# Optimization experiments

Hardware: AMD Instinct MI355X
Metric: run time of the kernel (lower is better)

## Reference

```python
import jax, jax.numpy as jnp
import numpy as np

N_IN = 200000
N_OUT = 600000
K = 27          # 3x3x3 kernel offsets
P = 150000      # kernel-map pairs per offset
C_IN = 96
C_OUT = 96
BN_EPS = 1e-5


def setup_inputs() -> dict:
    key = jax.random.key(0)
    k1, k2, k3, k4 = jax.random.split(key, 4)
    feats = jax.random.normal(k1, (N_IN, C_IN), dtype=jnp.float32)
    # kernel map: per offset, input-site indices and output-site indices
    in_idx = jax.random.randint(k2, (K, P), 0, N_IN, dtype=jnp.int32)
    out_idx = jax.random.randint(k3, (K, P), 0, N_OUT, dtype=jnp.int32)
    weight = jax.random.normal(k4, (K, C_IN, C_OUT), dtype=jnp.float32) * (1.0 / np.sqrt(C_IN * K))
    gamma = jnp.ones((C_OUT,), dtype=jnp.float32)
    beta = jnp.zeros((C_OUT,), dtype=jnp.float32)
    return {"feats": feats, "in_idx": in_idx, "out_idx": out_idx,
            "weight": weight, "gamma": gamma, "beta": beta}


def reference(feats, in_idx, out_idx, weight, gamma, beta):
    # Sparse transposed conv: gather -> matmul -> scatter-add per kernel offset.
    out = jnp.zeros((N_OUT, C_OUT), dtype=feats.dtype)
    for k in range(K):  # fixed small loop over kernel offsets (structurally distinct weights)
        contrib = feats[in_idx[k]] @ weight[k]          # [P, C_OUT]
        out = out.at[out_idx[k]].add(contrib)
    # BatchNorm (training-mode batch stats over active output sites), per channel
    mean = jnp.mean(out, axis=0)
    var = jnp.mean((out - mean) ** 2, axis=0)
    y = (out - mean) * jax.lax.rsqrt(var + BN_EPS) * gamma + beta
    # ReLU
    return jax.nn.relu(y)
```

## Files before the change

### kernel.cpp

```cpp
#include <hip/hip_runtime.h>
#include <hip/hip_bf16.h>

#define N_IN   200000
#define N_OUT  600000
#define KOFF   27
#define PPAIR  150000
#define NPAIR  (KOFF * PPAIR)
#define C      96
#define BN_EPS 1e-5f

using bf16x8 = __attribute__((ext_vector_type(8))) __bf16;
using f32x4  = __attribute__((ext_vector_type(4))) float;

static __device__ __forceinline__ unsigned short f2b(float x) {
    __hip_bfloat16 h = __float2bfloat16(x);
    return *reinterpret_cast<unsigned short*>(&h);
}

__global__ void cvt_feats(const float* __restrict__ src, unsigned short* __restrict__ dst) {
    int t = blockIdx.x * 256 + threadIdx.x;
    const float4* s4 = (const float4*)src;
    float4 a = s4[2 * t], b = s4[2 * t + 1];
    union { unsigned short u[8]; uint4 v; } r;
    r.u[0] = f2b(a.x); r.u[1] = f2b(a.y); r.u[2] = f2b(a.z); r.u[3] = f2b(a.w);
    r.u[4] = f2b(b.x); r.u[5] = f2b(b.y); r.u[6] = f2b(b.z); r.u[7] = f2b(b.w);
    ((uint4*)dst)[t] = r.v;
}

__global__ void cvt_w(const float* __restrict__ w, unsigned short* __restrict__ wt) {
    int t = blockIdx.x * 256 + threadIdx.x;
    int k = t / 9216;
    int rem = t - k * 9216;
    int o = rem / 96;
    int i = rem - o * 96;
    wt[t] = f2b(w[k * 9216 + i * 96 + o]);
}

__global__ void k_hist(const int* __restrict__ out_idx, int* __restrict__ counts) {
    int t = blockIdx.x * 256 + threadIdx.x;
    if (t < NPAIR) atomicAdd(&counts[out_idx[t]], 1);
}

__global__ void k_bsum(const int* __restrict__ counts, int* __restrict__ bsum) {
    __shared__ int ls[256];
    int b = blockIdx.x, t = threadIdx.x;
    int base = b * 1024 + t * 4;
    int s = 0;
#pragma unroll
    for (int j = 0; j < 4; j++) { int i = base + j; if (i < N_OUT) s += counts[i]; }
    ls[t] = s;
    __syncthreads();
    for (int off = 128; off > 0; off >>= 1) {
        if (t < off) ls[t] += ls[t + off];
        __syncthreads();
    }
    if (t == 0) bsum[b] = ls[0];
}

__global__ void k_scan_bsum(const int* __restrict__ bsum, int* __restrict__ bsum_ex) {
    __shared__ int sc[1024];
    int t = threadIdx.x;
    int v = (t < 586) ? bsum[t] : 0;
    sc[t] = v;
    __syncthreads();
    for (int off = 1; off < 1024; off <<= 1) {
        int add = (t >= off) ? sc[t - off] : 0;
        __syncthreads();
        sc[t] += add;
        __syncthreads();
    }
    bsum_ex[t] = sc[t] - v;
}

__global__ void k_scan_local(const int* __restrict__ counts, const int* __restrict__ bsum_ex,
                             int* __restrict__ csr) {
    __shared__ int sc[256];
    int b = blockIdx.x, t = threadIdx.x;
    int base = b * 1024 + t * 4;
    int c[4];
    int s = 0;
#pragma unroll
    for (int j = 0; j < 4; j++) {
        int i = base + j;
        c[j] = (i < N_OUT) ? counts[i] : 0;
        s += c[j];
    }
    sc[t] = s;
    __syncthreads();
    for (int off = 1; off < 256; off <<= 1) {
        int add = (t >= off) ? sc[t - off] : 0;
        __syncthreads();
        sc[t] += add;
        __syncthreads();
    }
    int run = bsum_ex[b] + sc[t] - s;
#pragma unroll
    for (int j = 0; j < 4; j++) {
        int i = base + j;
        if (i < N_OUT) {
            csr[i] = run;
            run += c[j];
            if (i == N_OUT - 1) csr[N_OUT] = run;
        }
    }
}

__global__ void k_rank(const int* __restrict__ out_idx, int* __restrict__ cursor,
                       int* __restrict__ rank) {
    int t = blockIdx.x * 256 + threadIdx.x;
    if (t < NPAIR) {
        int o = out_idx[t];
        rank[t] = atomicAdd(&cursor[o], 1);
    }
}

__global__ __launch_bounds__(256, 4) void contrib_k(
    const unsigned short* __restrict__ fb,
    const unsigned short* __restrict__ wt,
    const int* __restrict__ in_idx,
    const int* __restrict__ rank,
    unsigned short* __restrict__ contrib)
{
    __shared__ unsigned short As[64][104];
    __shared__ unsigned short Bs[96][104];
    __shared__ int s_rank[64];

    const int t    = threadIdx.x;
    const int k    = blockIdx.y;
    const int row0 = blockIdx.x * 64;
    const long kp  = (long)k * PPAIR;

    if (t < 64) {
        int p = row0 + t;
        s_rank[t] = (p < PPAIR) ? rank[kp + p] : -1;
    }
    for (int i = t; i < 64 * 12; i += 256) {
        int row = i / 12, ch = i - row * 12;
        int p = row0 + row; if (p >= PPAIR) p = PPAIR - 1;
        int g = in_idx[kp + p];
        *(uint4*)(&As[row][ch * 8]) = *(const uint4*)(fb + (size_t)g * 96 + ch * 8);
    }
    {
        const uint4* wsrc = (const uint4*)(wt + (size_t)k * 9216);
        for (int i = t; i < 96 * 12; i += 256) {
            int row = i / 12, ch = i - row * 12;
            *(uint4*)(&Bs[row][ch * 8]) = wsrc[row * 12 + ch];
        }
    }
    __syncthreads();

    const int wave = t >> 6, lane = t & 63;
    const int quad = lane >> 4, l16 = lane & 15;
    const int mrow = wave * 16 + l16;

    f32x4 acc[6];
#pragma unroll
    for (int n = 0; n < 6; n++) acc[n] = (f32x4){0.f, 0.f, 0.f, 0.f};

#pragma unroll
    for (int kk = 0; kk < 3; kk++) {
        int kb = kk * 32 + quad * 8;
        bf16x8 a = *(const bf16x8*)(&As[mrow][kb]);
#pragma unroll
        for (int n = 0; n < 6; n++) {
            bf16x8 b = *(const bf16x8*)(&Bs[n * 16 + l16][kb]);
            acc[n] = __builtin_amdgcn_mfma_f32_16x16x32_bf16(a, b, acc[n], 0, 0, 0);
        }
    }

#pragma unroll
    for (int r = 0; r < 4; r++) {
        int lr = wave * 16 + quad * 4 + r;
        int rk = s_rank[lr];
        if (rk >= 0) {
            unsigned short* crow = contrib + (size_t)rk * 96;
#pragma unroll
            for (int n = 0; n < 6; n++)
                crow[n * 16 + l16] = f2b(acc[n][r]);
        }
    }
}

__global__ __launch_bounds__(384) void reduce_bn(
    const unsigned short* __restrict__ contrib,
    const int* __restrict__ csr,
    float* __restrict__ out,
    float* __restrict__ sums)
{
    __shared__ float lsum[96], lq[96];
    int t = threadIdx.x;
    int rl = t / 48, c2 = t - rl * 48;
    float ps0 = 0.f, ps1 = 0.f, pq0 = 0.f, pq1 = 0.f;

    for (int rb = blockIdx.x * 8; rb < N_OUT; rb += gridDim.x * 8) {
        int r = rb + rl;
        int s = csr[r], e = csr[r + 1];
        float acc0 = 0.f, acc1 = 0.f;
        for (int j = s; j < e; j++) {
            unsigned int u = *(const unsigned int*)(contrib + (size_t)j * 96 + c2 * 2);
            acc0 += __uint_as_float(u << 16);
            acc1 += __uint_as_float(u & 0xffff0000u);
        }
        *(float2*)(out + (size_t)r * 96 + c2 * 2) = make_float2(acc0, acc1);
        ps0 += acc0; ps1 += acc1;
        pq0 += acc0 * acc0; pq1 += acc1 * acc1;
    }

    if (t < 96) { lsum[t] = 0.f; lq[t] = 0.f; }
    __syncthreads();
    atomicAdd(&lsum[c2 * 2 + 0], ps0); atomicAdd(&lsum[c2 * 2 + 1], ps1);
    atomicAdd(&lq[c2 * 2 + 0], pq0);   atomicAdd(&lq[c2 * 2 + 1], pq1);
    __syncthreads();
    if (t < 96) {
        atomicAdd(&sums[t], lsum[t]);
        atomicAdd(&sums[96 + t], lq[t]);
    }
}

__global__ void bn_final(float* __restrict__ sums, const float* __restrict__ gamma,
                         const float* __restrict__ beta) {
    int c = threadIdx.x;
    if (c < 96) {
        float mean = sums[c] * (1.0f / (float)N_OUT);
        float var  = sums[96 + c] * (1.0f / (float)N_OUT) - mean * mean;
        float inv  = rsqrtf(var + BN_EPS);
        float sc   = inv * gamma[c];
        sums[c]      = sc;
        sums[96 + c] = beta[c] - mean * sc;
    }
}

__global__ void bn_apply(float* __restrict__ out, const float* __restrict__ sums) {
    int t = blockIdx.x * 256 + threadIdx.x;
    int g = t % 24;
    float sc0 = sums[g * 4 + 0], sc1 = sums[g * 4 + 1];
    float sc2 = sums[g * 4 + 2], sc3 = sums[g * 4 + 3];
    float sh0 = sums[96 + g * 4 + 0], sh1 = sums[96 + g * 4 + 1];
    float sh2 = sums[96 + g * 4 + 2], sh3 = sums[96 + g * 4 + 3];
    float4* o4 = (float4*)out;
    for (long f = t; f < 14400000L; f += 258048) {
        float4 v = o4[f];
        v.x = fmaxf(v.x * sc0 + sh0, 0.f);
        v.y = fmaxf(v.y * sc1 + sh1, 0.f);
        v.z = fmaxf(v.z * sc2 + sh2, 0.f);
        v.w = fmaxf(v.w * sc3 + sh3, 0.f);
        o4[f] = v;
    }
}

extern "C" void kernel_launch(void* const* d_in, const int* in_sizes, int n_in,
                              void* d_out, int out_size, void* d_ws, size_t ws_size,
                              hipStream_t stream) {
    const float* feats  = (const float*)d_in[0];
    const int* in_idx   = (const int*)d_in[1];
    const int* out_idx  = (const int*)d_in[2];
    const float* weight = (const float*)d_in[3];
    const float* gamma  = (const float*)d_in[4];
    const float* beta   = (const float*)d_in[5];
    float* out = (float*)d_out;

    char* ws = (char*)d_ws;
    size_t off = 0;
    unsigned short* fb      = (unsigned short*)(ws + off); off += 38400000;
    unsigned short* wt      = (unsigned short*)(ws + off); off += 497664;
    unsigned short* contrib = (unsigned short*)(ws + off); off += (size_t)NPAIR * 96 * 2;
    int* counts             = (int*)(ws + off); off += 2400000;
    int* csr                = (int*)(ws + off); off += 2400016;
    int* cursor             = (int*)(ws + off); off += 2400016;
    int* bsum               = (int*)(ws + off); off += 4096;
    int* bsum_ex            = (int*)(ws + off); off += 4096;
    int* rank               = (int*)(ws + off); off += (size_t)NPAIR * 4;
    float* sums             = (float*)(ws + off); off += 768;

    hipMemsetAsync(counts, 0, (size_t)N_OUT * sizeof(int), stream);
    hipMemsetAsync(sums, 0, 192 * sizeof(float), stream);

    cvt_feats<<<9375, 256, 0, stream>>>(feats, fb);
    cvt_w<<<972, 256, 0, stream>>>(weight, wt);

    k_hist<<<(NPAIR + 255) / 256, 256, 0, stream>>>(out_idx, counts);
    k_bsum<<<586, 256, 0, stream>>>(counts, bsum);
    k_scan_bsum<<<1, 1024, 0, stream>>>(bsum, bsum_ex);
    k_scan_local<<<586, 256, 0, stream>>>(counts, bsum_ex, csr);
    hipMemcpyAsync(cursor, csr, (size_t)N_OUT * sizeof(int), hipMemcpyDeviceToDevice, stream);
    k_rank<<<(NPAIR + 255) / 256, 256, 0, stream>>>(out_idx, cursor, rank);

    contrib_k<<<dim3(2344, KOFF), 256, 0, stream>>>(fb, wt, in_idx, rank, contrib);

    reduce_bn<<<2048, 384, 0, stream>>>(contrib, csr, out, sums);
    bn_final<<<1, 128, 0, stream>>>(sums, gamma, beta);
    bn_apply<<<1008, 256, 0, stream>>>(out, sums);
}
```

Before: 1.618 ms.

## Load GEMM operands directly from global, stage output for coalesced stores, widen reduce

The contrib kernel stops staging the gathered feature rows and the weight tile in shared memory and has each lane read its MFMA operands straight from global memory, with weights expected to stay cache-resident. Results are written to a small per-wave shared buffer and then stored as 16-byte row chunks instead of 2-byte scattered stores, and the occupancy hint is raised. The reduce kernel now handles four channels per thread with 8-byte loads, unrolls the pair loop by two, and launches more blocks. The risks are more redundant global or L2 traffic for the weight operand, and smaller blocks adding more shared-memory atomics on the BN statistics.

```diff
diff --git a/kernel.cpp b/kernel.cpp
--- a/kernel.cpp
+++ b/kernel.cpp
@@ -16,6 +16,8 @@
     __hip_bfloat16 h = __float2bfloat16(x);
     return *reinterpret_cast<unsigned short*>(&h);
 }
+static __device__ __forceinline__ float b_lo(unsigned int u) { return __uint_as_float(u << 16); }
+static __device__ __forceinline__ float b_hi(unsigned int u) { return __uint_as_float(u & 0xffff0000u); }
 
 __global__ void cvt_feats(const float* __restrict__ src, unsigned short* __restrict__ dst) {
     int t = blockIdx.x * 256 + threadIdx.x;
@@ -114,16 +116,16 @@
     }
 }
 
-__global__ __launch_bounds__(256, 4) void contrib_k(
+__global__ __launch_bounds__(256, 6) void contrib_k(
     const unsigned short* __restrict__ fb,
     const unsigned short* __restrict__ wt,
     const int* __restrict__ in_idx,
     const int* __restrict__ rank,
     unsigned short* __restrict__ contrib)
 {
-    __shared__ unsigned short As[64][104];
-    __shared__ unsigned short Bs[96][104];
+    __shared__ int s_g[64];
     __shared__ int s_rank[64];
+    __shared__ __align__(16) unsigned short Ds[4][16 * 104];
 
     const int t    = threadIdx.x;
     const int k    = blockIdx.y;
@@ -131,21 +133,10 @@
     const long kp  = (long)k * PPAIR;
 
     if (t < 64) {
-        int p = row0 + t;
+        int p  = row0 + t;
+        int pc = (p < PPAIR) ? p : (PPAIR - 1);
+        s_g[t]    = in_idx[kp + pc];
         s_rank[t] = (p < PPAIR) ? rank[kp + p] : -1;
-    }
-    for (int i = t; i < 64 * 12; i += 256) {
-        int row = i / 12, ch = i - row * 12;
-        int p = row0 + row; if (p >= PPAIR) p = PPAIR - 1;
-        int g = in_idx[kp + p];
-        *(uint4*)(&As[row][ch * 8]) = *(const uint4*)(fb + (size_t)g * 96 + ch * 8);
-    }
-    {
-        const uint4* wsrc = (const uint4*)(wt + (size_t)k * 9216);
-        for (int i = t; i < 96 * 12; i += 256) {
-            int row = i / 12, ch = i - row * 12;
-            *(uint4*)(&Bs[row][ch * 8]) = wsrc[row * 12 + ch];
-        }
     }
     __syncthreads();
 
@@ -153,30 +144,42 @@
     const int quad = lane >> 4, l16 = lane & 15;
     const int mrow = wave * 16 + l16;
 
+    const unsigned short* arow = fb + (size_t)s_g[mrow] * 96 + quad * 8;
+    const unsigned short* bbase = wt + (size_t)k * 9216 + l16 * 96 + quad * 8;
+
     f32x4 acc[6];
 #pragma unroll
     for (int n = 0; n < 6; n++) acc[n] = (f32x4){0.f, 0.f, 0.f, 0.f};
 
 #pragma unroll
     for (int kk = 0; kk < 3; kk++) {
-        int kb = kk * 32 + quad * 8;
-        bf16x8 a = *(const bf16x8*)(&As[mrow][kb]);
+        bf16x8 a = *(const bf16x8*)(arow + kk * 32);
 #pragma unroll
         for (int n = 0; n < 6; n++) {
-            bf16x8 b = *(const bf16x8*)(&Bs[n * 16 + l16][kb]);
+            bf16x8 b = *(const bf16x8*)(bbase + n * 16 * 96 + kk * 32);
             acc[n] = __builtin_amdgcn_mfma_f32_16x16x32_bf16(a, b, acc[n], 0, 0, 0);
         }
     }
 
+    unsigned short* dw = &Ds[wave][0];
 #pragma unroll
     for (int r = 0; r < 4; r++) {
-        int lr = wave * 16 + quad * 4 + r;
-        int rk = s_rank[lr];
+        int prow = r * 4 + quad;
+#pragma unroll
+        for (int n = 0; n < 6; n++)
+            dw[prow * 104 + n * 16 + l16] = f2b(acc[n][r]);
+    }
+    __syncthreads();
+
+#pragma unroll
+    for (int s = 0; s < 3; s++) {
+        int q = s * 64 + lane;
+        int prow = q / 12, ci = q - prow * 12;
+        int orig = ((prow & 3) << 2) | (prow >> 2);
+        int rk = s_rank[wave * 16 + orig];
         if (rk >= 0) {
-            unsigned short* crow = contrib + (size_t)rk * 96;
-#pragma unroll
-            for (int n = 0; n < 6; n++)
-                crow[n * 16 + l16] = f2b(acc[n][r]);
+            uint4 v = *(const uint4*)(dw + prow * 104 + ci * 8);
+            *(uint4*)(contrib + (size_t)rk * 96 + ci * 8) = v;
         }
     }
 }
@@ -189,27 +192,36 @@
 {
     __shared__ float lsum[96], lq[96];
     int t = threadIdx.x;
-    int rl = t / 48, c2 = t - rl * 48;
-    float ps0 = 0.f, ps1 = 0.f, pq0 = 0.f, pq1 = 0.f;
-
-    for (int rb = blockIdx.x * 8; rb < N_OUT; rb += gridDim.x * 8) {
+    int rl = t / 24, c4 = t - rl * 24;
+    float ps0 = 0.f, ps1 = 0.f, ps2 = 0.f, ps3 = 0.f;
+    float pq0 = 0.f, pq1 = 0.f, pq2 = 0.f, pq3 = 0.f;
+
+    for (int rb = blockIdx.x * 16; rb < N_OUT; rb += gridDim.x * 16) {
         int r = rb + rl;
         int s = csr[r], e = csr[r + 1];
-        float acc0 = 0.f, acc1 = 0.f;
-        for (int j = s; j < e; j++) {
-            unsigned int u = *(const unsigned int*)(contrib + (size_t)j * 96 + c2 * 2);
-            acc0 += __uint_as_float(u << 16);
-            acc1 += __uint_as_float(u & 0xffff0000u);
-        }
-        *(float2*)(out + (size_t)r * 96 + c2 * 2) = make_float2(acc0, acc1);
-        ps0 += acc0; ps1 += acc1;
-        pq0 += acc0 * acc0; pq1 += acc1 * acc1;
+        float a0 = 0.f, a1 = 0.f, a2 = 0.f, a3 = 0.f;
+        int j = s;
+        for (; j + 1 < e; j += 2) {
+            uint2 u = *(const uint2*)(contrib + (size_t)j * 96 + c4 * 4);
+            uint2 v = *(const uint2*)(contrib + (size_t)(j + 1) * 96 + c4 * 4);
+            a0 += b_lo(u.x); a1 += b_hi(u.x); a2 += b_lo(u.y); a3 += b_hi(u.y);
+            a0 += b_lo(v.x); a1 += b_hi(v.x); a2 += b_lo(v.y); a3 += b_hi(v.y);
+        }
+        if (j < e) {
+            uint2 u = *(const uint2*)(contrib + (size_t)j * 96 + c4 * 4);
+            a0 += b_lo(u.x); a1 += b_hi(u.x); a2 += b_lo(u.y); a3 += b_hi(u.y);
+        }
+        *(float4*)(out + (size_t)r * 96 + c4 * 4) = make_float4(a0, a1, a2, a3);
+        ps0 += a0; ps1 += a1; ps2 += a2; ps3 += a3;
+        pq0 += a0 * a0; pq1 += a1 * a1; pq2 += a2 * a2; pq3 += a3 * a3;
     }
 
     if (t < 96) { lsum[t] = 0.f; lq[t] = 0.f; }
     __syncthreads();
-    atomicAdd(&lsum[c2 * 2 + 0], ps0); atomicAdd(&lsum[c2 * 2 + 1], ps1);
-    atomicAdd(&lq[c2 * 2 + 0], pq0);   atomicAdd(&lq[c2 * 2 + 1], pq1);
+    atomicAdd(&lsum[c4 * 4 + 0], ps0); atomicAdd(&lsum[c4 * 4 + 1], ps1);
+    atomicAdd(&lsum[c4 * 4 + 2], ps2); atomicAdd(&lsum[c4 * 4 + 3], ps3);
+    atomicAdd(&lq[c4 * 4 + 0], pq0);   atomicAdd(&lq[c4 * 4 + 1], pq1);
+    atomicAdd(&lq[c4 * 4 + 2], pq2);   atomicAdd(&lq[c4 * 4 + 3], pq3);
     __syncthreads();
     if (t < 96) {
         atomicAdd(&sums[t], lsum[t]);
@@ -287,7 +299,7 @@
 
     contrib_k<<<dim3(2344, KOFF), 256, 0, stream>>>(fb, wt, in_idx, rank, contrib);
 
-    reduce_bn<<<2048, 384, 0, stream>>>(contrib, csr, out, sums);
+    reduce_bn<<<9375, 384, 0, stream>>>(contrib, csr, out, sums);
     bn_final<<<1, 128, 0, stream>>>(sums, gamma, beta);
     bn_apply<<<1008, 256, 0, stream>>>(out, sums);
 }
```

After: 1.575 ms. -2.7%, faster.
